# Optimization experiments

Hardware: AMD Instinct MI355X
Metric: run time of the kernel (lower is better)

The kernel has to match this reference:

```python
import jax, jax.numpy as jnp
import numpy as np

WIDTH = 384
STEP_SIZE = 0.1  # hard-coded in EnergyBlock.__init__
EPS = 1e-5


def conv1d(x, w):
    # x: [B, Cin, L], w: [Cout, Cin, K], stride 1, SAME padding (padding=1 for k=3)
    return jax.lax.conv_general_dilated(
        x, w, window_strides=(1,), padding='SAME',
        dimension_numbers=('NCH', 'OIH', 'NCH'))


def layer_norm_cl(x):
    # torch layer_norm over shape[1:] == normalize jointly over (C, L) per batch elem,
    # no affine params, biased variance.
    mu = jnp.mean(x, axis=(1, 2), keepdims=True)
    var = jnp.mean(jnp.square(x - mu), axis=(1, 2), keepdims=True)
    return (x - mu) * jax.lax.rsqrt(var + EPS)


def energy_block(cat, op_w):
    # cat: [B, width+1, L] = concat(interim_thought, x)
    xl = layer_norm_cl(cat[:, :WIDTH])          # post-LN x (the grad variable)
    c = conv1d(cat, op_w)                        # operator(inputs): no path through xl
    # Ex = sum(c * xl) + sum(where(xl>=0, xl^2, 0))
    # dEx/dxl = c + 2*relu(xl)  (analytic; matches torch.autograd.grad)
    grads = c + 2.0 * jnp.maximum(xl, 0.0)
    return xl - STEP_SIZE * grads


def _init_conv(key, cout, cin, k=3):
    scale = (1.0 / (cin * k)) ** 0.5
    return jax.random.uniform(key, (cout, cin, k), jnp.float32, -scale, scale)


def setup_inputs() -> dict:
    key = jax.random.key(0)
    ks = jax.random.split(key, 6)
    B, L = 32, 512
    return {
        'x': jax.random.normal(ks[0], (B, 1, L), jnp.float32),
        'iters_to_do': 16,
        'proj_w': _init_conv(ks[1], WIDTH, 1),
        'op_w': _init_conv(ks[2], WIDTH, WIDTH + 1),
        'h1_w': _init_conv(ks[3], WIDTH, WIDTH),
        'h2_w': _init_conv(ks[4], WIDTH // 2, WIDTH),
        'h3_w': _init_conv(ks[5], 2, WIDTH // 2),
    }


def reference(x, iters_to_do, proj_w, op_w, h1_w, h2_w, h3_w):
    relu = jax.nn.relu
    interim = relu(conv1d(x, proj_w))  # initial_thought [B, width, L]

    def step(it, _):
        cat = jnp.concatenate([it, x], axis=1)       # recall=True
        new_it = energy_block(cat, op_w)
        out = conv1d(relu(conv1d(relu(conv1d(new_it, h1_w)), h2_w)), h3_w)  # [B,2,L]
        return new_it, out

    _, outs = jax.lax.scan(step, interim, None, length=iters_to_do)
    # eval mode: return all_outputs [B, iters, 2, L]
    return jnp.transpose(outs, (1, 0, 2, 3))
```

## Files before the change

kernel.cpp:

```cpp
#include <hip/hip_runtime.h>
#include <hip/hip_bf16.h>

#define BB 32
#define WW 384
#define LL 512
#define ITERS 16
#define NPB (WW * LL)
#define LROWS 514
#define RP (LROWS * 8)

typedef __attribute__((ext_vector_type(8))) short bf16x8;
typedef __attribute__((ext_vector_type(4))) float f32x4;

__device__ __forceinline__ float b2f(short s) {
    unsigned u = ((unsigned)(unsigned short)s) << 16;
    float f;
    __builtin_memcpy(&f, &u, 4);
    return f;
}
__device__ __forceinline__ short f2b(float v) {
    __hip_bfloat16 h = __float2bfloat16(v);
    return *(short*)&h;
}

__device__ __forceinline__ void gld16(const short* g, short* l) {
    __builtin_amdgcn_global_load_lds(
        (const __attribute__((address_space(1))) unsigned int*)g,
        (__attribute__((address_space(3))) unsigned int*)l, 16, 0, 0);
}

__global__ void wsplit_op(const float* __restrict__ w, short* __restrict__ wh) {
    int i = blockIdx.x * 256 + threadIdx.x;
    if (i >= 3 * 48 * 384 * 8) return;
    int e = i & 7, co = (i >> 3) % 384, oct = (i >> 3) / 384 % 48,
        tap = i / (8 * 384 * 48);
    int ci = oct * 8 + e;
    wh[i] = f2b(w[(co * 385 + ci) * 3 + tap]);
}

__global__ void wx_prep(const float* __restrict__ w, float* __restrict__ wx) {
    int i = blockIdx.x * 256 + threadIdx.x;
    if (i >= 3 * 384) return;
    int co = i % 384, tap = i / 384;
    wx[tap * 384 + co] = w[(co * 385 + 384) * 3 + tap];
}

__global__ void wsplit_h(const float* __restrict__ w, short* __restrict__ wh,
                         int COD, int CO_real) {
    int i = blockIdx.x * 256 + threadIdx.x;
    if (i >= 3 * 48 * COD * 8) return;
    int e = i & 7, co = (i >> 3) % COD, oct = (i >> 3) / COD % 48,
        tap = i / (8 * COD * 48);
    int ci = oct * 8 + e;
    float v = (co < CO_real) ? w[(co * 384 + ci) * 3 + tap] : 0.f;
    wh[i] = f2b(v);
}

__global__ void init_rows(short* itAh, short* itAl, short* itBh, short* itBl,
                          short* a1A, short* a1B, short* a2A, short* a2B) {
    int row = (blockIdx.x & 1) ? (LROWS - 1) : 0;
    int b = blockIdx.x >> 1;
    int tid = threadIdx.x;
    for (int i = tid; i < 48 * 8; i += 64) {
        size_t o = (size_t)b * 48 * RP + (size_t)(i >> 3) * RP + row * 8 + (i & 7);
        itAh[o] = 0; itAl[o] = 0; itBh[o] = 0; itBl[o] = 0;
        a1A[o] = 0; a1B[o] = 0;
    }
    for (int i = tid; i < 24 * 8; i += 64) {
        size_t o = (size_t)b * 24 * RP + (size_t)(i >> 3) * RP + row * 8 + (i & 7);
        a2A[o] = 0; a2B[o] = 0;
    }
}

__global__ void zero_part(float* part, int n) {
    int i = blockIdx.x * 256 + threadIdx.x;
    if (i < n) part[i] = 0.f;
}

__global__ __launch_bounds__(256) void proj_relu(const float* __restrict__ x,
                                                 const float* __restrict__ wp,
                                                 short* __restrict__ oh,
                                                 short* __restrict__ ol,
                                                 float* __restrict__ part) {
    int low3 = blockIdx.x & 7, r0 = blockIdx.x >> 3;
    int sl_lo = r0 & 3, chi = r0 >> 2;
    int c3 = chi * 8 + low3;
    int b = c3 >> 1, sl = ((c3 & 1) << 2) | sl_lo;
    int tid = threadIdx.x;
    __shared__ float ws[WW * 3];
    __shared__ float xs[66];
    for (int i = tid; i < WW * 3; i += 256) ws[i] = wp[i];
    int l0 = sl * 64;
    for (int i = tid; i < 66; i += 256) {
        int l = l0 + i - 1;
        xs[i] = (l >= 0 && l < LL) ? x[b * LL + l] : 0.f;
    }
    __syncthreads();
    size_t sb = (size_t)b * 48 * RP;
    float s = 0.f, sq = 0.f;
    for (int idx = tid; idx < 64 * WW; idx += 256) {
        int lo = idx / WW, co = idx % WW;
        float v = fmaxf(ws[co * 3] * xs[lo] + ws[co * 3 + 1] * xs[lo + 1] +
                            ws[co * 3 + 2] * xs[lo + 2], 0.f);
        size_t o = sb + (size_t)(co >> 3) * RP + (l0 + lo + 1) * 8 + (co & 7);
        __hip_bfloat16 h = __float2bfloat16(v);
        oh[o] = *(short*)&h;
        ol[o] = f2b(v - __bfloat162float(h));
        s += v; sq += v * v;
    }
    #pragma unroll
    for (int off = 32; off > 0; off >>= 1) {
        s += __shfl_down(s, off);
        sq += __shfl_down(sq, off);
    }
    __shared__ float sr[8];
    int w = tid >> 6;
    if ((tid & 63) == 0) { sr[w] = s; sr[4 + w] = sq; }
    __syncthreads();
    if (tid == 0) {
        atomicAdd(&part[b * 2], sr[0] + sr[1] + sr[2] + sr[3]);
        atomicAdd(&part[b * 2 + 1], sr[4] + sr[5] + sr[6] + sr[7]);
    }
}


#define PIPE_BARRIER()                                                     \
    do {                                                                   \
        asm volatile("s_waitcnt vmcnt(8)" ::: "memory");                   \
        __builtin_amdgcn_sched_barrier(0);                                 \
        __builtin_amdgcn_s_barrier();                                      \
        __builtin_amdgcn_sched_barrier(0);                                 \
    } while (0)

#define MMAC(A, B, MT, NT)                                                 \
    acc[MT][NT] = __builtin_amdgcn_mfma_f32_16x16x32_bf16(A, B,            \
                                                          acc[MT][NT], 0, 0, 0);

#define STAGE(KC, TB)                                                      \
    do {                                                                   \
        short* sb_ = smem + (TB) * ASZ;                                    \
        _Pragma("unroll")                                                  \
        for (int r_ = 0; r_ < (ANS + 3) / 4; r_++) {                       \
            int s_ = r_ * 4 + wn;                                          \
            if (s_ < ANS) {                                                \
                int u0_ = s_ * 64;                                         \
                if (u0_ > AU - 64) u0_ = AU - 64;                          \
                int u_ = u0_ + lane;                                       \
                int oc_ = u_ / TLROWS;                                     \
                int rw_ = u_ - oc_ * TLROWS;                               \
                gld16(inh + ibase + (size_t)((KC) * 4 + oc_) * RP +        \
                          (size_t)(l0 + rw_) * 8,                          \
                      sb_ + u0_ * 8);                                      \
            }                                                              \
        }                                                                  \
    } while (0)

#define DECL_B(S) bf16x8 fb0##S, fb1##S, fb2##S, fb3##S;

#define LOADB(S, T, KC)                                                    \
    do {                                                                   \
        const short* bp_ = wh + ((((size_t)(T) * CHUNKS + (KC)) * 4 + q) * \
                                     COD + co0w + lane15) * 8;             \
        fb0##S = *(const bf16x8*)(bp_);                                    \
        fb1##S = *(const bf16x8*)(bp_ + 16 * 8);                           \
        fb2##S = *(const bf16x8*)(bp_ + 32 * 8);                           \
        fb3##S = *(const bf16x8*)(bp_ + 48 * 8);                           \
    } while (0)

#define COMP_TAP(SB, T, S)                                                 \
    do {                                                                   \
        const short* As_ = (SB);                                           \
        int ar_ = q * TLROWS + wl + lane15 + (T);                          \
        bf16x8 fa0 = *(const bf16x8*)(As_ + ar_ * 8);                      \
        bf16x8 fa1 = *(const bf16x8*)(As_ + (ar_ + 16) * 8);               \
        bf16x8 fa2 = *(const bf16x8*)(As_ + (ar_ + 32) * 8);               \
        bf16x8 fa3 = *(const bf16x8*)(As_ + (ar_ + 48) * 8);               \
        MMAC(fa0, fb0##S, 0, 0) MMAC(fa0, fb1##S, 0, 1)                    \
        MMAC(fa0, fb2##S, 0, 2) MMAC(fa0, fb3##S, 0, 3)                    \
        MMAC(fa1, fb0##S, 1, 0) MMAC(fa1, fb1##S, 1, 1)                    \
        MMAC(fa1, fb2##S, 1, 2) MMAC(fa1, fb3##S, 1, 3)                    \
        MMAC(fa2, fb0##S, 2, 0) MMAC(fa2, fb1##S, 2, 1)                    \
        MMAC(fa2, fb2##S, 2, 2) MMAC(fa2, fb3##S, 2, 3)                    \
        MMAC(fa3, fb0##S, 3, 0) MMAC(fa3, fb1##S, 3, 1)                    \
        MMAC(fa3, fb2##S, 3, 2) MMAC(fa3, fb3##S, 3, 3)                    \
    } while (0)

template <int CHUNKS, int IOCT, int OOCT, int COD, int MODE, int LSPLIT>
__device__ __forceinline__ void conv_body(
    int bid, short* smem,
    const short* __restrict__ inh, const short* __restrict__ inl,
    const short* __restrict__ wh, const float* __restrict__ xf,
    const float* __restrict__ wx, const float* __restrict__ part_in,
    float* __restrict__ part_out, short* __restrict__ outh,
    short* __restrict__ outl) {
    constexpr int TLROWS = LSPLIT ? 258 : 130;
    constexpr int ASZ = 4 * TLROWS * 8;
    constexpr int AU = 4 * TLROWS;
    constexpr int ANS = (AU + 63) / 64;

    int tid = threadIdx.x;
    int lane = tid & 63;
    int wn = __builtin_amdgcn_readfirstlane(tid >> 6);
    int lane15 = lane & 15, q = lane >> 4;
    int b, l0, co0, wl, wco;
    if (LSPLIT) {
        int low3 = bid & 7, r0 = bid >> 3;
        int ct = r0 % 3, chi = r0 / 3;
        int c2 = chi * 8 + low3;
        b = c2 >> 1; l0 = (c2 & 1) * 256; co0 = ct * 64;
        wl = wn * 64; wco = 0;
    } else {
        int low3 = bid & 7, r0 = bid >> 3;
        int ct = r0 % 3, s2 = r0 / 3;
        int ltlo = s2 & 1, chi = s2 >> 1;
        int c = chi * 8 + low3;
        b = c >> 1;
        int lt = ((c & 1) << 1) | ltlo;
        l0 = lt * 128; co0 = ct * 128;
        wl = (wn >> 1) * 64; wco = (wn & 1) * 64;
    }
    const int co0w = co0 + wco;
    const size_t ibase = (size_t)b * IOCT * RP;

    f32x4 acc[4][4];
    #pragma unroll
    for (int i = 0; i < 4; i++)
        #pragma unroll
        for (int j = 0; j < 4; j++) acc[i][j] = (f32x4){0.f, 0.f, 0.f, 0.f};

    DECL_B(X)
    DECL_B(Y)
    DECL_B(Z)
    STAGE(0, 0);
    LOADB(X, 0, 0);
    LOADB(Y, 1, 0);
    PIPE_BARRIER();
    #pragma unroll 2
    for (int kc = 0; kc < CHUNKS; kc++) {
        int cur = kc & 1;
        LOADB(Z, 2, kc);
        if (kc + 1 < CHUNKS) STAGE(kc + 1, cur ^ 1);
        short* sb = smem + cur * ASZ;
        COMP_TAP(sb, 0, X);
        if (kc + 1 < CHUNKS) LOADB(X, 0, kc + 1);
        COMP_TAP(sb, 1, Y);
        if (kc + 1 < CHUNKS) LOADB(Y, 1, kc + 1);
        COMP_TAP(sb, 2, Z);
        PIPE_BARRIER();
    }

    int l0w = l0 + wl;
    const size_t obase = (size_t)b * OOCT * RP;
    if constexpr (MODE == 1) {
        float s_in = part_in[b * 2], sq_in = part_in[b * 2 + 1];
        float mu = s_in / (float)NPB;
        float var = sq_in / (float)NPB - mu * mu;
        float rs = rsqrtf(var + 1e-5f);
        const float* xb = xf + b * LL;
        float s = 0.f, sq = 0.f;
        #pragma unroll
        for (int nt = 0; nt < 4; nt++) {
            int n = co0w + nt * 16 + lane15;
            float w0 = wx[n], w1 = wx[384 + n], w2 = wx[768 + n];
            #pragma unroll
            for (int mt = 0; mt < 4; mt++)
                #pragma unroll
                for (int r = 0; r < 4; r++) {
                    int m = mt * 16 + q * 4 + r;
                    int l = l0w + m;
                    size_t idx = ibase + (size_t)(n >> 3) * RP +
                                 (l + 1) * 8 + (n & 7);
                    float xm1 = (l > 0) ? xb[l - 1] : 0.f;
                    float xp1 = (l < LL - 1) ? xb[l + 1] : 0.f;
                    float c = acc[mt][nt][r] + w0 * xm1 + w1 * xb[l] + w2 * xp1;
                    float itv = b2f(inh[idx]) + b2f(inl[idx]);
                    float xl = (itv - mu) * rs;
                    float nv = xl - 0.1f * c - 0.2f * fmaxf(xl, 0.f);
                    s += nv;
                    sq += nv * nv;
                    __hip_bfloat16 h = __float2bfloat16(nv);
                    outh[idx] = *(short*)&h;
                    outl[idx] = f2b(nv - __bfloat162float(h));
                }
        }
        #pragma unroll
        for (int off = 32; off > 0; off >>= 1) {
            s += __shfl_down(s, off);
            sq += __shfl_down(sq, off);
        }
        __shared__ float sr[8];
        if (lane == 0) { sr[wn] = s; sr[4 + wn] = sq; }
        __syncthreads();
        if (tid == 0) {
            atomicAdd(&part_out[b * 2], sr[0] + sr[1] + sr[2] + sr[3]);
            atomicAdd(&part_out[b * 2 + 1], sr[4] + sr[5] + sr[6] + sr[7]);
        }
    } else {
        #pragma unroll
        for (int mt = 0; mt < 4; mt++)
            #pragma unroll
            for (int nt = 0; nt < 4; nt++)
                #pragma unroll
                for (int r = 0; r < 4; r++) {
                    int m = mt * 16 + q * 4 + r;
                    int n = co0w + nt * 16 + lane15;
                    size_t idx = obase + (size_t)(n >> 3) * RP +
                                 (l0w + m + 1) * 8 + (n & 7);
                    outh[idx] = f2b(fmaxf(acc[mt][nt][r], 0.f));
                }
    }
}

__device__ __forceinline__ void h3_body(int bid, short* smem,
                                        const short* __restrict__ a2,
                                        const float* __restrict__ w3,
                                        float* __restrict__ out, int t) {
    float* ws3 = (float*)smem;
    int tid = threadIdx.x;
    for (int i = tid; i < 2 * 192 * 3; i += 256) ws3[i] = w3[i];
    __syncthreads();
    int low3 = bid & 7, r0 = bid >> 3;
    int qlo = r0 & 1, chi = r0 >> 1;
    int c = chi * 8 + low3;
    int b = c >> 1;
    int qq = ((c & 1) << 1) | qlo;
    int l = qq * 128 + (tid >> 1);
    int ch = tid & 1;
    const short* ab = a2 + (size_t)b * 24 * RP;
    const float* wc = ws3 + ch * 576;
    float a = 0.f;
    #pragma unroll 4
    for (int oct = 0; oct < 24; oct++) {
        const short* p = ab + (size_t)oct * RP + l * 8;
        bf16x8 v0 = *(const bf16x8*)p;
        bf16x8 v1 = *(const bf16x8*)(p + 8);
        bf16x8 v2 = *(const bf16x8*)(p + 16);
        #pragma unroll
        for (int j = 0; j < 8; j++) {
            const float* wp = wc + (oct * 8 + j) * 3;
            a += wp[0] * b2f(v0[j]) + wp[1] * b2f(v1[j]) + wp[2] * b2f(v2[j]);
        }
    }
    out[(((size_t)b * ITERS + t) * 2 + ch) * LL + l] = a;
}

__global__ __launch_bounds__(256, 3) void fusedF(
    const short* __restrict__ ch, const short* __restrict__ cl,
    short* __restrict__ nh, short* __restrict__ nl,
    const short* __restrict__ wOph, const short* __restrict__ wH1,
    const short* __restrict__ wH2, const float* __restrict__ xf,
    const float* __restrict__ wx, const float* __restrict__ part_in,
    float* __restrict__ part_out, short* __restrict__ a1w,
    const short* __restrict__ a1r, short* __restrict__ a2w,
    const short* __restrict__ a2r, const float* __restrict__ w3,
    float* __restrict__ out, int th3, int opB, int h1B, int h2B) {
    __shared__ __align__(16) short smem[2 * 4 * 258 * 8];
    int bid = blockIdx.x;
    if (bid < opB) {
        conv_body<12, 48, 48, 384, 1, 0>(bid, smem, ch, cl, wOph, xf, wx,
                                         part_in, part_out, nh, nl);
    } else if (bid < opB + h1B) {
        conv_body<12, 48, 48, 384, 0, 0>(bid - opB, smem, ch, nullptr, wH1,
                                         nullptr, nullptr, nullptr, nullptr,
                                         a1w, nullptr);
    } else if (bid < opB + h1B + h2B) {
        conv_body<12, 48, 24, 192, 0, 1>(bid - opB - h1B, smem, a1r, nullptr,
                                         wH2, nullptr, nullptr, nullptr,
                                         nullptr, a2w, nullptr);
    } else {
        h3_body(bid - opB - h1B - h2B, smem, a2r, w3, out, th3);
    }
}

extern "C" void kernel_launch(void* const* d_in, const int* in_sizes, int n_in,
                              void* d_out, int out_size, void* d_ws, size_t ws_size,
                              hipStream_t stream) {
    const float* x = (const float*)d_in[0];
    const float* proj_w = (const float*)d_in[2];
    const float* op_w = (const float*)d_in[3];
    const float* h1_w = (const float*)d_in[4];
    const float* h2_w = (const float*)d_in[5];
    const float* h3_w = (const float*)d_in[6];
    float* out = (float*)d_out;

    char* base = (char*)d_ws;
    size_t off = 0;
    auto alloc = [&](size_t bytes) {
        char* p = base + off;
        off += (bytes + 255) & ~(size_t)255;
        return p;
    };
    const size_t ITB = (size_t)BB * 48 * RP * 2;
    short* itAh = (short*)alloc(ITB);
    short* itAl = (short*)alloc(ITB);
    short* itBh = (short*)alloc(ITB);
    short* itBl = (short*)alloc(ITB);
    short* a1A = (short*)alloc((size_t)BB * 48 * RP * 2);
    short* a1B = (short*)alloc((size_t)BB * 48 * RP * 2);
    short* a2A = (short*)alloc((size_t)BB * 24 * RP * 2);
    short* a2B = (short*)alloc((size_t)BB * 24 * RP * 2);
    short* wOph = (short*)alloc((size_t)3 * 48 * 384 * 8 * 2);
    short* wH1 = (short*)alloc((size_t)3 * 48 * 384 * 8 * 2);
    short* wH2 = (short*)alloc((size_t)3 * 48 * 192 * 8 * 2);
    float* wx = (float*)alloc((size_t)3 * 384 * 4);
    float* part = (float*)alloc((size_t)(ITERS + 1) * 64 * 4);
    if (off > ws_size) return;

    wsplit_op<<<(3 * 48 * 384 * 8 + 255) / 256, 256, 0, stream>>>(op_w, wOph);
    wx_prep<<<5, 256, 0, stream>>>(op_w, wx);
    wsplit_h<<<(3 * 48 * 384 * 8 + 255) / 256, 256, 0, stream>>>(h1_w, wH1, 384, 384);
    wsplit_h<<<(3 * 48 * 192 * 8 + 255) / 256, 256, 0, stream>>>(h2_w, wH2, 192, 192);
    init_rows<<<BB * 2, 64, 0, stream>>>(itAh, itAl, itBh, itBl, a1A, a1B,
                                         a2A, a2B);
    zero_part<<<5, 256, 0, stream>>>(part, (ITERS + 1) * 64);
    proj_relu<<<BB * 8, 256, 0, stream>>>(x, proj_w, itAh, itAl, part);

    short* a1buf[2] = {a1A, a1B};
    short* a2buf[2] = {a2A, a2B};
    short *ch = itAh, *cl = itAl, *nh = itBh, *nl = itBl;
    for (int t = 0; t < ITERS + 3; t++) {
        int opB = (t < ITERS) ? 384 : 0;
        int h1B = (t >= 1 && t <= ITERS) ? 384 : 0;
        int h2B = (t >= 2 && t <= ITERS + 1) ? 192 : 0;
        int h3B = (t >= 3 && t <= ITERS + 2) ? 128 : 0;
        int tp = (t < ITERS) ? t : 0;
        fusedF<<<opB + h1B + h2B + h3B, 256, 0, stream>>>(
            ch, cl, nh, nl, wOph, wH1, wH2, x, wx, part + tp * 64,
            part + (tp + 1) * 64, a1buf[(t - 1) & 1], a1buf[(t - 2) & 1],
            a2buf[(t - 2) & 1], a2buf[(t + 1) & 1], h3_w, out, t - 3,
            opB, h1B, h2B);
        if (t < ITERS) {
            short* th = ch; ch = nh; nh = th;
            short* tl = cl; cl = nl; nl = tl;
        }
    }
}
```

Baseline: 953.6 us.

## Stage eight input octets per barrier and merge prep kernels into one launch

The conv main loop now stages a group of 8 input octets (two K-chunks) per LDS buffer for the op and h1 convolutions. It spreads the staging loads for the next group across the sub-chunks and places a barrier only once per group, which halves the number of block-wide barriers. Separately, the six small setup kernels (weight splits, wx prep, row zeroing, part zeroing) are merged into a single prep launch to cut launch overhead. LDS usage stays about the same. The larger groups change the pipeline depth and halve the number of prefetch points.

```diff
diff --git a/kernel.cpp b/kernel.cpp
--- a/kernel.cpp
+++ b/kernel.cpp
@@ -29,52 +29,53 @@
         (__attribute__((address_space(3))) unsigned int*)l, 16, 0, 0);
 }
 
-__global__ void wsplit_op(const float* __restrict__ w, short* __restrict__ wh) {
-    int i = blockIdx.x * 256 + threadIdx.x;
-    if (i >= 3 * 48 * 384 * 8) return;
-    int e = i & 7, co = (i >> 3) % 384, oct = (i >> 3) / 384 % 48,
-        tap = i / (8 * 384 * 48);
-    int ci = oct * 8 + e;
-    wh[i] = f2b(w[(co * 385 + ci) * 3 + tap]);
-}
-
-__global__ void wx_prep(const float* __restrict__ w, float* __restrict__ wx) {
-    int i = blockIdx.x * 256 + threadIdx.x;
-    if (i >= 3 * 384) return;
-    int co = i % 384, tap = i / 384;
-    wx[tap * 384 + co] = w[(co * 385 + 384) * 3 + tap];
-}
-
-__global__ void wsplit_h(const float* __restrict__ w, short* __restrict__ wh,
-                         int COD, int CO_real) {
-    int i = blockIdx.x * 256 + threadIdx.x;
-    if (i >= 3 * 48 * COD * 8) return;
-    int e = i & 7, co = (i >> 3) % COD, oct = (i >> 3) / COD % 48,
-        tap = i / (8 * COD * 48);
-    int ci = oct * 8 + e;
-    float v = (co < CO_real) ? w[(co * 384 + ci) * 3 + tap] : 0.f;
-    wh[i] = f2b(v);
-}
-
-__global__ void init_rows(short* itAh, short* itAl, short* itBh, short* itBl,
-                          short* a1A, short* a1B, short* a2A, short* a2B) {
-    int row = (blockIdx.x & 1) ? (LROWS - 1) : 0;
-    int b = blockIdx.x >> 1;
-    int tid = threadIdx.x;
-    for (int i = tid; i < 48 * 8; i += 64) {
-        size_t o = (size_t)b * 48 * RP + (size_t)(i >> 3) * RP + row * 8 + (i & 7);
-        itAh[o] = 0; itAl[o] = 0; itBh[o] = 0; itBl[o] = 0;
-        a1A[o] = 0; a1B[o] = 0;
-    }
-    for (int i = tid; i < 24 * 8; i += 64) {
-        size_t o = (size_t)b * 24 * RP + (size_t)(i >> 3) * RP + row * 8 + (i & 7);
-        a2A[o] = 0; a2B[o] = 0;
-    }
-}
-
-__global__ void zero_part(float* part, int n) {
-    int i = blockIdx.x * 256 + threadIdx.x;
-    if (i < n) part[i] = 0.f;
+__global__ __launch_bounds__(256) void prep(
+    const float* __restrict__ op_w, const float* __restrict__ h1_w,
+    const float* __restrict__ h2_w, short* __restrict__ wOph,
+    short* __restrict__ wH1, short* __restrict__ wH2, float* __restrict__ wx,
+    short* itAh, short* itAl, short* itBh, short* itBl,
+    short* a1A, short* a1B, short* a2A, short* a2B, float* part) {
+    int bid = blockIdx.x, tid = threadIdx.x;
+    if (bid < 1728) {
+        int i = bid * 256 + tid;
+        int e = i & 7, co = (i >> 3) % 384, oct = (i >> 3) / 384 % 48,
+            tap = i / (8 * 384 * 48);
+        wOph[i] = f2b(op_w[(co * 385 + oct * 8 + e) * 3 + tap]);
+    } else if (bid < 3456) {
+        int i = (bid - 1728) * 256 + tid;
+        int e = i & 7, co = (i >> 3) % 384, oct = (i >> 3) / 384 % 48,
+            tap = i / (8 * 384 * 48);
+        wH1[i] = f2b(h1_w[(co * 384 + oct * 8 + e) * 3 + tap]);
+    } else if (bid < 4320) {
+        int i = (bid - 3456) * 256 + tid;
+        int e = i & 7, co = (i >> 3) % 192, oct = (i >> 3) / 192 % 48,
+            tap = i / (8 * 192 * 48);
+        wH2[i] = f2b(h2_w[(co * 384 + oct * 8 + e) * 3 + tap]);
+    } else if (bid < 4325) {
+        int i = (bid - 4320) * 256 + tid;
+        if (i < 3 * 384) {
+            int co = i % 384, tap = i / 384;
+            wx[tap * 384 + co] = op_w[(co * 385 + 384) * 3 + tap];
+        }
+    } else if (bid < 4330) {
+        int i = (bid - 4325) * 256 + tid;
+        if (i < (ITERS + 1) * 64) part[i] = 0.f;
+    } else {
+        int rb = bid - 4330;
+        int row = (rb & 1) ? (LROWS - 1) : 0;
+        int b = rb >> 1;
+        for (int i = tid; i < 48 * 8; i += 256) {
+            size_t o = (size_t)b * 48 * RP + (size_t)(i >> 3) * RP +
+                       row * 8 + (i & 7);
+            itAh[o] = 0; itAl[o] = 0; itBh[o] = 0; itBl[o] = 0;
+            a1A[o] = 0; a1B[o] = 0;
+        }
+        for (int i = tid; i < 24 * 8; i += 256) {
+            size_t o = (size_t)b * 24 * RP + (size_t)(i >> 3) * RP +
+                       row * 8 + (i & 7);
+            a2A[o] = 0; a2B[o] = 0;
+        }
+    }
 }
 
 __global__ __launch_bounds__(256) void proj_relu(const float* __restrict__ x,
@@ -136,19 +137,19 @@
     acc[MT][NT] = __builtin_amdgcn_mfma_f32_16x16x32_bf16(A, B,            \
                                                           acc[MT][NT], 0, 0, 0);
 
-#define STAGE(KC, TB)                                                      \
+#define STAGE_R(KG, TB, S0, S1)                                            \
     do {                                                                   \
         short* sb_ = smem + (TB) * ASZ;                                    \
         _Pragma("unroll")                                                  \
-        for (int r_ = 0; r_ < (ANS + 3) / 4; r_++) {                       \
-            int s_ = r_ * 4 + wn;                                          \
-            if (s_ < ANS) {                                                \
+        for (int r_ = 0; r_ < ((S1) - (S0) + 3) / 4; r_++) {               \
+            int s_ = (S0) + r_ * 4 + wn;                                   \
+            if (s_ < (S1)) {                                               \
                 int u0_ = s_ * 64;                                         \
                 if (u0_ > AU - 64) u0_ = AU - 64;                          \
                 int u_ = u0_ + lane;                                       \
                 int oc_ = u_ / TLROWS;                                     \
                 int rw_ = u_ - oc_ * TLROWS;                               \
-                gld16(inh + ibase + (size_t)((KC) * 4 + oc_) * RP +        \
+                gld16(inh + ibase + (size_t)((KG) * GOCT + oc_) * RP +     \
                           (size_t)(l0 + rw_) * 8,                          \
                       sb_ + u0_ * 8);                                      \
             }                                                              \
@@ -167,10 +168,10 @@
         fb3##S = *(const bf16x8*)(bp_ + 48 * 8);                           \
     } while (0)
 
-#define COMP_TAP(SB, T, S)                                                 \
+#define COMP_TAP(SB, OG, T, S)                                             \
     do {                                                                   \
         const short* As_ = (SB);                                           \
-        int ar_ = q * TLROWS + wl + lane15 + (T);                          \
+        int ar_ = ((OG) * 4 + q) * TLROWS + wl + lane15 + (T);             \
         bf16x8 fa0 = *(const bf16x8*)(As_ + ar_ * 8);                      \
         bf16x8 fa1 = *(const bf16x8*)(As_ + (ar_ + 16) * 8);               \
         bf16x8 fa2 = *(const bf16x8*)(As_ + (ar_ + 32) * 8);               \
@@ -185,7 +186,8 @@
         MMAC(fa3, fb2##S, 3, 2) MMAC(fa3, fb3##S, 3, 3)                    \
     } while (0)
 
-template <int CHUNKS, int IOCT, int OOCT, int COD, int MODE, int LSPLIT>
+template <int CHUNKS, int IOCT, int OOCT, int COD, int MODE, int LSPLIT,
+          int GOCT>
 __device__ __forceinline__ void conv_body(
     int bid, short* smem,
     const short* __restrict__ inh, const short* __restrict__ inl,
@@ -194,9 +196,12 @@
     float* __restrict__ part_out, short* __restrict__ outh,
     short* __restrict__ outl) {
     constexpr int TLROWS = LSPLIT ? 258 : 130;
-    constexpr int ASZ = 4 * TLROWS * 8;
-    constexpr int AU = 4 * TLROWS;
+    constexpr int SUBS = GOCT / 4;
+    constexpr int NG = CHUNKS / SUBS;
+    constexpr int ASZ = GOCT * TLROWS * 8;
+    constexpr int AU = GOCT * TLROWS;
     constexpr int ANS = (AU + 63) / 64;
+    constexpr int SPS = (ANS + SUBS - 1) / SUBS;
 
     int tid = threadIdx.x;
     int lane = tid & 63;
@@ -231,21 +236,29 @@
     DECL_B(X)
     DECL_B(Y)
     DECL_B(Z)
-    STAGE(0, 0);
+    STAGE_R(0, 0, 0, ANS);
     LOADB(X, 0, 0);
     LOADB(Y, 1, 0);
     PIPE_BARRIER();
     #pragma unroll 2
-    for (int kc = 0; kc < CHUNKS; kc++) {
-        int cur = kc & 1;
-        LOADB(Z, 2, kc);
-        if (kc + 1 < CHUNKS) STAGE(kc + 1, cur ^ 1);
+    for (int g = 0; g < NG; g++) {
+        int cur = g & 1;
         short* sb = smem + cur * ASZ;
-        COMP_TAP(sb, 0, X);
-        if (kc + 1 < CHUNKS) LOADB(X, 0, kc + 1);
-        COMP_TAP(sb, 1, Y);
-        if (kc + 1 < CHUNKS) LOADB(Y, 1, kc + 1);
-        COMP_TAP(sb, 2, Z);
+        #pragma unroll
+        for (int s = 0; s < SUBS; s++) {
+            int kc = g * SUBS + s;
+            LOADB(Z, 2, kc);
+            if (g + 1 < NG) {
+                int s0 = s * SPS;
+                int s1 = (s0 + SPS > ANS) ? ANS : s0 + SPS;
+                STAGE_R(g + 1, cur ^ 1, s0, s1);
+            }
+            COMP_TAP(sb, s, 0, X);
+            if (kc + 1 < CHUNKS) LOADB(X, 0, kc + 1);
+            COMP_TAP(sb, s, 1, Y);
+            if (kc + 1 < CHUNKS) LOADB(Y, 1, kc + 1);
+            COMP_TAP(sb, s, 2, Z);
+        }
         PIPE_BARRIER();
     }
 
@@ -354,19 +367,19 @@
     const short* __restrict__ a1r, short* __restrict__ a2w,
     const short* __restrict__ a2r, const float* __restrict__ w3,
     float* __restrict__ out, int th3, int opB, int h1B, int h2B) {
-    __shared__ __align__(16) short smem[2 * 4 * 258 * 8];
+    __shared__ __align__(16) short smem[2 * 8 * 130 * 8];
     int bid = blockIdx.x;
     if (bid < opB) {
-        conv_body<12, 48, 48, 384, 1, 0>(bid, smem, ch, cl, wOph, xf, wx,
-                                         part_in, part_out, nh, nl);
+        conv_body<12, 48, 48, 384, 1, 0, 8>(bid, smem, ch, cl, wOph, xf, wx,
+                                            part_in, part_out, nh, nl);
     } else if (bid < opB + h1B) {
-        conv_body<12, 48, 48, 384, 0, 0>(bid - opB, smem, ch, nullptr, wH1,
-                                         nullptr, nullptr, nullptr, nullptr,
-                                         a1w, nullptr);
+        conv_body<12, 48, 48, 384, 0, 0, 8>(bid - opB, smem, ch, nullptr,
+                                            wH1, nullptr, nullptr, nullptr,
+                                            nullptr, a1w, nullptr);
     } else if (bid < opB + h1B + h2B) {
-        conv_body<12, 48, 24, 192, 0, 1>(bid - opB - h1B, smem, a1r, nullptr,
-                                         wH2, nullptr, nullptr, nullptr,
-                                         nullptr, a2w, nullptr);
+        conv_body<12, 48, 24, 192, 0, 1, 4>(bid - opB - h1B, smem, a1r,
+                                            nullptr, wH2, nullptr, nullptr,
+                                            nullptr, nullptr, a2w, nullptr);
     } else {
         h3_body(bid - opB - h1B - h2B, smem, a2r, w3, out, th3);
     }
@@ -406,13 +419,9 @@
     float* part = (float*)alloc((size_t)(ITERS + 1) * 64 * 4);
     if (off > ws_size) return;
 
-    wsplit_op<<<(3 * 48 * 384 * 8 + 255) / 256, 256, 0, stream>>>(op_w, wOph);
-    wx_prep<<<5, 256, 0, stream>>>(op_w, wx);
-    wsplit_h<<<(3 * 48 * 384 * 8 + 255) / 256, 256, 0, stream>>>(h1_w, wH1, 384, 384);
-    wsplit_h<<<(3 * 48 * 192 * 8 + 255) / 256, 256, 0, stream>>>(h2_w, wH2, 192, 192);
-    init_rows<<<BB * 2, 64, 0, stream>>>(itAh, itAl, itBh, itBl, a1A, a1B,
-                                         a2A, a2B);
-    zero_part<<<5, 256, 0, stream>>>(part, (ITERS + 1) * 64);
+    prep<<<4394, 256, 0, stream>>>(op_w, h1_w, h2_w, wOph, wH1, wH2, wx,
+                                   itAh, itAl, itBh, itBl, a1A, a1B, a2A,
+                                   a2B, part);
     proj_relu<<<BB * 8, 256, 0, stream>>>(x, proj_w, itAh, itAl, part);
 
     short* a1buf[2] = {a1A, a1B};
```

Result: no change. 940.4 us (median of 2 runs) (-1.4%).
